# Kernel tuning notes

Measured on AMD Instinct MI355X. Metric: run time of the kernel, lower is better.

The kernel has to match this reference:

```python
import jax, jax.numpy as jnp
import numpy as np

D = 1024      # d_model
H = 16        # num_heads
DK = D // H   # head dim = 64
C = 64        # chunk_size
MRP = 2 * C   # max_rel_pos = 128
B, S = 2, 2048


def setup_inputs() -> dict:
    key = jax.random.key(0)
    ks = jax.random.split(key, 7)
    s = 0.02
    x = jax.random.normal(ks[0], (B, S, D), jnp.float32)
    Wq = jax.random.normal(ks[1], (D, D), jnp.float32) * s
    Wk = jax.random.normal(ks[2], (D, D), jnp.float32) * s
    Wv = jax.random.normal(ks[3], (D, D), jnp.float32) * s
    Wo = jax.random.normal(ks[4], (D, D), jnp.float32) * s
    bq = jnp.zeros((D,), jnp.float32)
    bk = jnp.zeros((D,), jnp.float32)
    bv = jnp.zeros((D,), jnp.float32)
    bo = jnp.zeros((D,), jnp.float32)
    # torch init is zeros; use small values so the bias path is exercised
    rel_bias = jax.random.normal(ks[5], (2 * MRP + 1, H), jnp.float32) * s
    return dict(x=x, Wq=Wq, bq=bq, Wk=Wk, bk=bk, Wv=Wv, bv=bv, Wo=Wo, bo=bo,
                rel_bias=rel_bias)


def reference(x, Wq, bq, Wk, bk, Wv, bv, Wo, bo, rel_bias):
    b, s, _ = x.shape

    def heads(w, bias):
        return (x @ w + bias).reshape(b, s, H, DK).transpose(0, 2, 1, 3)  # [B,H,S,dk]

    Q = heads(Wq, bq)
    K = heads(Wk, bk)
    V = heads(Wv, bv)

    scale = jnp.sqrt(jnp.asarray(DK, x.dtype))
    scores = jnp.einsum('bhqd,bhkd->bhqk', Q, K) / scale  # [B,H,S,S]

    pos = jnp.arange(s)
    # chunked path's rel index reduces to global (q - k), clamped
    rel = jnp.clip(pos[:, None] - pos[None, :], -MRP, MRP) + MRP  # [S,S]
    bias2 = rel_bias[rel].transpose(2, 0, 1)  # [H,S,S]
    scores = scores + bias2[None]

    # growing-window chunk mask: query chunk i sees key chunks 0..i
    qc = pos // C
    allowed = qc[None, :] <= qc[:, None]  # [S_q, S_k]
    scores = jnp.where(allowed[None, None], scores, -jnp.inf)

    attn = jax.nn.softmax(scores, axis=-1)
    out = jnp.einsum('bhqk,bhkd->bhqd', attn, V)
    out = out.transpose(0, 2, 1, 3).reshape(b, s, D)
    return out @ Wo + bo
```

## Files before the change

### kernel.cpp

```cpp
#include <hip/hip_runtime.h>
#include <stdint.h>

#define NH 16
#define DKH 64
#define SEQ 2048
#define NBATCH 2
#define NROW (NBATCH*SEQ)
#define DM 1024
#define LOG2E 1.44269504088896f

typedef __attribute__((ext_vector_type(8))) __bf16 bf16x8;
typedef __attribute__((ext_vector_type(4))) __bf16 bf16x4;
typedef __attribute__((ext_vector_type(4))) float f32x4;

#if __has_builtin(__builtin_amdgcn_exp2f)
#define EXP2(x) __builtin_amdgcn_exp2f(x)
#else
#define EXP2(x) exp2f(x)
#endif

__device__ __forceinline__ unsigned short f2bf(float f) {
  union { float f; uint32_t u; } v; v.f = f;
  uint32_t r = v.u + 0x7FFFu + ((v.u >> 16) & 1u);
  return (unsigned short)(r >> 16);
}
__device__ __forceinline__ f32x4 mfma16(bf16x8 a, bf16x8 b, f32x4 c) {
  return __builtin_amdgcn_mfma_f32_16x16x32_bf16(a, b, c, 0, 0, 0);
}
__device__ __forceinline__ void gload_lds16(const void* g, void* l) {
  __builtin_amdgcn_global_load_lds(
      (__attribute__((address_space(1))) uint32_t*)(uintptr_t)g,
      (__attribute__((address_space(3))) uint32_t*)(uintptr_t)l,
      16, 0, 0);
}
__device__ __forceinline__ void barrier_raw() {
  asm volatile("" ::: "memory");
  __builtin_amdgcn_s_barrier();
  asm volatile("" ::: "memory");
}

__global__ __launch_bounds__(256) void k_cvt_x(const float* __restrict__ x,
                                               unsigned short* __restrict__ xb) {
  int i = blockIdx.x * 256 + threadIdx.x;
  float4 v = ((const float4*)x)[i];
  ushort4 o;
  o.x = f2bf(v.x); o.y = f2bf(v.y); o.z = f2bf(v.z); o.w = f2bf(v.w);
  ((ushort4*)xb)[i] = o;
}

__global__ __launch_bounds__(256) void k_cvt_w(
    const float* __restrict__ Wq, const float* __restrict__ Wk,
    const float* __restrict__ Wv, const float* __restrict__ Wo,
    unsigned short* __restrict__ Wqt, unsigned short* __restrict__ Wkt,
    unsigned short* __restrict__ Wvt, unsigned short* __restrict__ Wot) {
  __shared__ float tile[32][33];
  int z = blockIdx.z;
  const float* W = (z == 0) ? Wq : (z == 1) ? Wk : (z == 2) ? Wv : Wo;
  int ti = blockIdx.x, tj = blockIdx.y;
  int c = threadIdx.x & 31, r0 = threadIdx.x >> 5;
#pragma unroll
  for (int rr = 0; rr < 4; ++rr) {
    int r = r0 + rr * 8;
    tile[r][c] = W[(ti * 32 + r) * DM + tj * 32 + c];
  }
  __syncthreads();
  unsigned short* Out = (z == 0) ? Wqt : (z == 1) ? Wkt : (z == 2) ? Wvt : Wot;
#pragma unroll
  for (int rr = 0; rr < 4; ++rr) {
    int a = r0 + rr * 8;
    float v = tile[c][a];
    Out[(tj * 32 + a) * DM + ti * 32 + c] = f2bf(v);
  }
}

__global__ __launch_bounds__(256) void k_gemm_qkv(
    const unsigned short* __restrict__ xb,
    const unsigned short* __restrict__ Wqt, const unsigned short* __restrict__ Wkt,
    const unsigned short* __restrict__ Wvt,
    const float* __restrict__ bq, const float* __restrict__ bk,
    const float* __restrict__ bv,
    unsigned short* __restrict__ Q, unsigned short* __restrict__ Ko,
    unsigned short* __restrict__ Vt) {
  __shared__ __align__(16) unsigned short Al[2][128 * 64];
  __shared__ __align__(16) unsigned short Bl[2][128 * 64];
  int z = blockIdx.z;
  const unsigned short* Wt = (z == 0) ? Wqt : (z == 1) ? Wkt : Wvt;
  const float* bias = (z == 0) ? bq : (z == 1) ? bk : bv;

  int m0 = blockIdx.x * 128, n0 = blockIdx.y * 128;
  int tid = threadIdx.x, lane = tid & 63, wave = tid >> 6;
  int wr = wave >> 1, wc = wave & 1;
  int l15 = lane & 15, lg = lane >> 4;
  int r3 = lane >> 3, s3 = lane & 7;
  int gsw = (s3 ^ r3) << 4;
  int swz = l15 & 7;

  f32x4 acc[4][4] = {};

  auto stage = [&](int kb, int b) {
#pragma unroll
    for (int c = 0; c < 4; ++c) {
      int rb = c * 32 + wave * 8;
      gload_lds16((const char*)xb + (size_t)(m0 + rb + r3) * 2048 + kb * 128 + gsw,
                  (char*)&Al[b][0] + rb * 128);
      gload_lds16((const char*)Wt + (size_t)(n0 + rb + r3) * 2048 + kb * 128 + gsw,
                  (char*)&Bl[b][0] + rb * 128);
    }
  };

  stage(0, 0);
  stage(1, 1);

  for (int kb = 0; kb < 16; ++kb) {
    if (kb < 15) asm volatile("s_waitcnt vmcnt(8)" ::: "memory");
    else         asm volatile("s_waitcnt vmcnt(0)" ::: "memory");
    barrier_raw();
    int b = kb & 1;
#pragma unroll
    for (int ks = 0; ks < 2; ++ks) {
      int slot = lg + 4 * ks;
      int sofs = ((slot ^ swz) << 4);
      bf16x8 a[4], bfr[4];
#pragma unroll
      for (int mt = 0; mt < 4; ++mt)
        a[mt] = *(const bf16x8*)((const char*)&Al[b][0] + (wr * 64 + mt * 16 + l15) * 128 + sofs);
#pragma unroll
      for (int nt = 0; nt < 4; ++nt)
        bfr[nt] = *(const bf16x8*)((const char*)&Bl[b][0] + (wc * 64 + nt * 16 + l15) * 128 + sofs);
#pragma unroll
      for (int mt = 0; mt < 4; ++mt)
#pragma unroll
        for (int nt = 0; nt < 4; ++nt)
          acc[mt][nt] = mfma16(a[mt], bfr[nt], acc[mt][nt]);
    }
    barrier_raw();
    if (kb < 14) stage(kb + 2, b);
  }

#pragma unroll
  for (int nt = 0; nt < 4; ++nt) {
    int n = n0 + wc * 64 + nt * 16 + l15;
    float bb = bias[n];
    int h = n >> 6, dk = n & 63;
#pragma unroll
    for (int mt = 0; mt < 4; ++mt) {
      int mbase = m0 + wr * 64 + mt * 16 + lg * 4;
      int bidx = mbase >> 11, s = mbase & 2047;
      if (z < 2) {
        unsigned short* Out = (z == 0) ? Q : Ko;
#pragma unroll
        for (int r = 0; r < 4; ++r)
          Out[(((size_t)(bidx * NH + h)) * SEQ + s + r) * DKH + dk] =
              f2bf(acc[mt][nt][r] + bb);
      } else {
        ushort4 pk;
        pk.x = f2bf(acc[mt][nt][0] + bb);
        pk.y = f2bf(acc[mt][nt][1] + bb);
        pk.z = f2bf(acc[mt][nt][2] + bb);
        pk.w = f2bf(acc[mt][nt][3] + bb);
        *(ushort4*)&Vt[((size_t)(bidx * NH + h) * DKH + dk) * SEQ + s] = pk;
      }
    }
  }
}

__global__ __launch_bounds__(256) void k_attn(
    const unsigned short* __restrict__ Qg, const unsigned short* __restrict__ Kg,
    const unsigned short* __restrict__ Vtg, const float* __restrict__ rel_bias,
    unsigned short* __restrict__ AOh) {
  __shared__ __align__(16) unsigned short Kl[2][64 * 64];
  __shared__ __align__(16) unsigned short Vl[2][64 * 64];
  __shared__ float biasl[257];

  int blk = blockIdx.x;
  int bh = blk & 31;
  int g = blk >> 5;
  int qc = (g < 16) ? (31 - g) : (g - 16);
  int h = bh & 15, bidx = bh >> 4;
  int tid = threadIdx.x, lane = tid & 63, wave = tid >> 6;
  int l15 = lane & 15, lg = lane >> 4;
  int r3 = lane >> 3, s3 = lane & 7;
  int gsw = (s3 ^ r3) * 16;

  const float C1L = 0.125f * LOG2E;

  for (int i = tid; i < 257; i += 256)
    biasl[i] = rel_bias[i * NH + h] * LOG2E - 6.0f * LOG2E;

  int qrow = qc * 64 + wave * 16 + l15;
  const unsigned short* qptr = Qg + ((size_t)bh * SEQ + qrow) * DKH + lg * 8;
  bf16x8 qf0 = *(const bf16x8*)(qptr);
  bf16x8 qf1 = *(const bf16x8*)(qptr + 32);

  const char* kcb = (const char*)(Kg + (size_t)bh * SEQ * DKH);
  const char* vcb = (const char*)(Vtg + (size_t)bh * DKH * SEQ);

  auto stage = [&](int j, int b) {
    const char* kj = kcb + (size_t)j * (64 * DKH * 2);
    const char* vj = vcb + (size_t)j * 128;
#pragma unroll
    for (int c = 0; c < 2; ++c) {
      int rb = wave * 16 + c * 8;
      gload_lds16(kj + (size_t)(rb + r3) * 128 + gsw,
                  (char*)&Kl[b][0] + rb * 128);
      gload_lds16(vj + (size_t)(rb + r3) * (SEQ * 2) + gsw,
                  (char*)&Vl[b][0] + rb * 128);
    }
  };

  f32x4 acc[4] = {};
  f32x4 accl = {};
  bf16x8 ones;
#pragma unroll
  for (int jj = 0; jj < 8; ++jj) ones[jj] = (__bf16)1.0f;

  float cfar = rel_bias[256 * NH + h] * LOG2E - 6.0f * LOG2E;
  int swz = (l15 & 7);

  int vo[4];
#pragma unroll
  for (int kt = 0; kt < 4; ++kt)
    vo[kt] = (((kt * 2 + (lg >> 1)) ^ swz) << 4) + ((lg & 1) << 3);

  stage(0, 0);
  asm volatile("s_waitcnt vmcnt(0)" ::: "memory");
  barrier_raw();

  for (int j = 0; j <= qc; ++j) {
    int cur = j & 1;
    if (j < qc) stage(j + 1, cur ^ 1);

    const char* Kc = (const char*)&Kl[cur][0];
    const char* Vc = (const char*)&Vl[cur][0];

    f32x4 sa[4] = {};
    __builtin_amdgcn_s_setprio(1);
#pragma unroll
    for (int ks = 0; ks < 2; ++ks) {
      bf16x8 qa = ks ? qf1 : qf0;
      int slot = lg + 4 * ks;
#pragma unroll
      for (int kt = 0; kt < 4; ++kt) {
        bf16x8 kfr = *(const bf16x8*)(Kc + (kt * 16 + l15) * 128 + ((slot ^ swz) * 16));
        sa[kt] = mfma16(kfr, qa, sa[kt]);
      }
    }
    __builtin_amdgcn_s_setprio(0);

    float p[4][4];
    if (j >= qc - 2) {
      int kb0 = j * 64 + lg * 4;
#pragma unroll
      for (int kt = 0; kt < 4; ++kt)
#pragma unroll
        for (int r = 0; r < 4; ++r) {
          int rel = qrow - (kb0 + kt * 16 + r);
          rel = min(max(rel, -128), 128) + 128;
          p[kt][r] = EXP2(fmaf(sa[kt][r], C1L, biasl[rel]));
        }
    } else {
#pragma unroll
      for (int kt = 0; kt < 4; ++kt)
#pragma unroll
        for (int r = 0; r < 4; ++r)
          p[kt][r] = EXP2(fmaf(sa[kt][r], C1L, cfar));
    }

    bf16x8 pfr0, pfr1;
#pragma unroll
    for (int jj = 0; jj < 4; ++jj) {
      pfr0[jj]     = (__bf16)p[0][jj];
      pfr0[jj + 4] = (__bf16)p[1][jj];
      pfr1[jj]     = (__bf16)p[2][jj];
      pfr1[jj + 4] = (__bf16)p[3][jj];
    }

    __builtin_amdgcn_s_setprio(1);
#pragma unroll
    for (int dt = 0; dt < 4; ++dt) {
      const char* vrow = Vc + (dt * 16 + l15) * 128;
      uint2 t0 = *(const uint2*)(vrow + vo[0]);
      uint2 t1 = *(const uint2*)(vrow + vo[1]);
      uint2 t2 = *(const uint2*)(vrow + vo[2]);
      uint2 t3 = *(const uint2*)(vrow + vo[3]);
      uint4 w0, w1;
      w0.x = t0.x; w0.y = t0.y; w0.z = t1.x; w0.w = t1.y;
      w1.x = t2.x; w1.y = t2.y; w1.z = t3.x; w1.w = t3.y;
      acc[dt] = mfma16(pfr0, *(const bf16x8*)&w0, acc[dt]);
      acc[dt] = mfma16(pfr1, *(const bf16x8*)&w1, acc[dt]);
    }
    accl = mfma16(pfr0, ones, accl);
    accl = mfma16(pfr1, ones, accl);
    __builtin_amdgcn_s_setprio(0);

    if (j < qc) {
      asm volatile("s_waitcnt vmcnt(0)" ::: "memory");
      barrier_raw();
    }
  }

#pragma unroll
  for (int r = 0; r < 4; ++r) {
    float inv = 1.0f / accl[r];
    int s = qc * 64 + wave * 16 + lg * 4 + r;
    size_t row = (size_t)bidx * SEQ + s;
#pragma unroll
    for (int dt = 0; dt < 4; ++dt) {
      float v = acc[dt][r] * inv;
      int col = h * 64 + dt * 16 + l15;
      AOh[row * DM + col] = f2bf(v);
    }
  }
}

__global__ __launch_bounds__(256) void k_gemm_out(
    const unsigned short* __restrict__ Ab, const unsigned short* __restrict__ Bt,
    const float* __restrict__ bo, float* __restrict__ out) {
  __shared__ __align__(16) unsigned short Al[2][64 * 64];
  __shared__ __align__(16) unsigned short Bl[2][128 * 64];

  int m0 = blockIdx.x * 64, n0 = blockIdx.y * 128;
  int tid = threadIdx.x, lane = tid & 63, wave = tid >> 6;
  int wr = wave >> 1, wc = wave & 1;
  int l15 = lane & 15, lg = lane >> 4;
  int r3 = lane >> 3, s3 = lane & 7;
  int gsw = (s3 ^ r3) << 4;
  int swz = l15 & 7;

  f32x4 acc[2][4] = {};

  auto stage = [&](int kb, int b) {
#pragma unroll
    for (int c = 0; c < 2; ++c) {
      int rb = c * 32 + wave * 8;
      gload_lds16((const char*)Ab + (size_t)(m0 + rb + r3) * 2048 + kb * 128 + gsw,
                  (char*)&Al[b][0] + rb * 128);
    }
#pragma unroll
    for (int c = 0; c < 4; ++c) {
      int rb = c * 32 + wave * 8;
      gload_lds16((const char*)Bt + (size_t)(n0 + rb + r3) * 2048 + kb * 128 + gsw,
                  (char*)&Bl[b][0] + rb * 128);
    }
  };

  stage(0, 0);
  stage(1, 1);

  for (int kb = 0; kb < 16; ++kb) {
    if (kb < 15) asm volatile("s_waitcnt vmcnt(6)" ::: "memory");
    else         asm volatile("s_waitcnt vmcnt(0)" ::: "memory");
    barrier_raw();
    int b = kb & 1;
#pragma unroll
    for (int ks = 0; ks < 2; ++ks) {
      int slot = lg + 4 * ks;
      int sofs = ((slot ^ swz) << 4);
      bf16x8 a[2], bfr[4];
#pragma unroll
      for (int mt = 0; mt < 2; ++mt)
        a[mt] = *(const bf16x8*)((const char*)&Al[b][0] + (wr * 32 + mt * 16 + l15) * 128 + sofs);
#pragma unroll
      for (int nt = 0; nt < 4; ++nt)
        bfr[nt] = *(const bf16x8*)((const char*)&Bl[b][0] + (wc * 64 + nt * 16 + l15) * 128 + sofs);
#pragma unroll
      for (int mt = 0; mt < 2; ++mt)
#pragma unroll
        for (int nt = 0; nt < 4; ++nt)
          acc[mt][nt] = mfma16(a[mt], bfr[nt], acc[mt][nt]);
    }
    barrier_raw();
    if (kb < 14) stage(kb + 2, b);
  }

#pragma unroll
  for (int nt = 0; nt < 4; ++nt) {
    int n = n0 + wc * 64 + nt * 16 + l15;
    float bb = bo[n];
#pragma unroll
    for (int mt = 0; mt < 2; ++mt) {
      int mbase = m0 + wr * 32 + mt * 16 + lg * 4;
#pragma unroll
      for (int r = 0; r < 4; ++r)
        out[(size_t)(mbase + r) * DM + n] = acc[mt][nt][r] + bb;
    }
  }
}

extern "C" void kernel_launch(void* const* d_in, const int* in_sizes, int n_in,
                              void* d_out, int out_size, void* d_ws, size_t ws_size,
                              hipStream_t stream) {
  const float* x  = (const float*)d_in[0];
  const float* Wq = (const float*)d_in[1];
  const float* bq = (const float*)d_in[2];
  const float* Wk = (const float*)d_in[3];
  const float* bk = (const float*)d_in[4];
  const float* Wv = (const float*)d_in[5];
  const float* bv = (const float*)d_in[6];
  const float* Wo = (const float*)d_in[7];
  const float* bo = (const float*)d_in[8];
  const float* rb = (const float*)d_in[9];
  float* out = (float*)d_out;

  char* ws = (char*)d_ws;
  size_t off = 0;
  auto alloc = [&](size_t bytes) {
    char* p = ws + off; off += (bytes + 255) & ~(size_t)255; return p;
  };
  unsigned short* xb   = (unsigned short*)alloc((size_t)NROW * DM * 2);
  unsigned short* Wqt  = (unsigned short*)alloc((size_t)DM * DM * 2);
  unsigned short* Wkt  = (unsigned short*)alloc((size_t)DM * DM * 2);
  unsigned short* Wvt  = (unsigned short*)alloc((size_t)DM * DM * 2);
  unsigned short* Wot  = (unsigned short*)alloc((size_t)DM * DM * 2);
  unsigned short* Qb   = (unsigned short*)alloc((size_t)NROW * DM * 2);
  unsigned short* Kb   = (unsigned short*)alloc((size_t)NROW * DM * 2);
  unsigned short* Vtb  = (unsigned short*)alloc((size_t)NROW * DM * 2);
  unsigned short* AOh  = (unsigned short*)alloc((size_t)NROW * DM * 2);

  k_cvt_x<<<dim3(NROW * DM / 4 / 256), dim3(256), 0, stream>>>(x, xb);
  k_cvt_w<<<dim3(32, 32, 4), dim3(256), 0, stream>>>(Wq, Wk, Wv, Wo,
                                                     Wqt, Wkt, Wvt, Wot);
  k_gemm_qkv<<<dim3(32, 8, 3), dim3(256), 0, stream>>>(xb, Wqt, Wkt, Wvt,
                                                       bq, bk, bv, Qb, Kb, Vtb);
  k_attn<<<dim3(1024), dim3(256), 0, stream>>>(Qb, Kb, Vtb, rb, AOh);
  k_gemm_out<<<dim3(64, 8), dim3(256), 0, stream>>>(AOh, Wot, bo, out);
}
```

Before: 100.1 us.

## Process two query chunks per attention block, 32 query rows per wave

Each attention block now covers two adjacent query chunks (128 rows), and each wave handles 32 rows with two fragment sets, so every K/V tile staged into LDS serves twice as many queries. The grid is halved to 512 blocks and uses a new chunk-pair ordering. Waves assigned the lower chunk skip the final key chunk but still take part in the barriers. The cost is more registers per wave, fewer blocks to fill the CUs, and some idle waves on the last iteration.

```diff
diff --git a/kernel.cpp b/kernel.cpp
--- a/kernel.cpp
+++ b/kernel.cpp
@@ -175,22 +175,31 @@
   int blk = blockIdx.x;
   int bh = blk & 31;
   int g = blk >> 5;
-  int qc = (g < 16) ? (31 - g) : (g - 16);
+  int a = (g < 8) ? g : (23 - g);
   int h = bh & 15, bidx = bh >> 4;
-  int tid = threadIdx.x, lane = tid & 63, wave = tid >> 6;
+  int tid = threadIdx.x, lane = tid & 63, w = tid >> 6;
   int l15 = lane & 15, lg = lane >> 4;
   int r3 = lane >> 3, s3 = lane & 7;
   int gsw = (s3 ^ r3) * 16;
 
+  int myqc = 2 * a + (w >> 1);
+  int qsub = w & 1;
+  int qcmax = 2 * a + 1;
+  int qbase = myqc * 64 + qsub * 32;
+
   const float C1L = 0.125f * LOG2E;
 
   for (int i = tid; i < 257; i += 256)
     biasl[i] = rel_bias[i * NH + h] * LOG2E - 6.0f * LOG2E;
 
-  int qrow = qc * 64 + wave * 16 + l15;
-  const unsigned short* qptr = Qg + ((size_t)bh * SEQ + qrow) * DKH + lg * 8;
-  bf16x8 qf0 = *(const bf16x8*)(qptr);
-  bf16x8 qf1 = *(const bf16x8*)(qptr + 32);
+  bf16x8 qf[2][2];
+#pragma unroll
+  for (int f = 0; f < 2; ++f) {
+    const unsigned short* qptr =
+        Qg + ((size_t)bh * SEQ + qbase + f * 16 + l15) * DKH + lg * 8;
+    qf[f][0] = *(const bf16x8*)(qptr);
+    qf[f][1] = *(const bf16x8*)(qptr + 32);
+  }
 
   const char* kcb = (const char*)(Kg + (size_t)bh * SEQ * DKH);
   const char* vcb = (const char*)(Vtg + (size_t)bh * DKH * SEQ);
@@ -200,7 +209,7 @@
     const char* vj = vcb + (size_t)j * 128;
 #pragma unroll
     for (int c = 0; c < 2; ++c) {
-      int rb = wave * 16 + c * 8;
+      int rb = w * 16 + c * 8;
       gload_lds16(kj + (size_t)(rb + r3) * 128 + gsw,
                   (char*)&Kl[b][0] + rb * 128);
       gload_lds16(vj + (size_t)(rb + r3) * (SEQ * 2) + gsw,
@@ -208,8 +217,8 @@
     }
   };
 
-  f32x4 acc[4] = {};
-  f32x4 accl = {};
+  f32x4 acc[2][4] = {};
+  f32x4 accl[2] = {};
   bf16x8 ones;
 #pragma unroll
   for (int jj = 0; jj < 8; ++jj) ones[jj] = (__bf16)1.0f;
@@ -226,91 +235,107 @@
   asm volatile("s_waitcnt vmcnt(0)" ::: "memory");
   barrier_raw();
 
-  for (int j = 0; j <= qc; ++j) {
+  for (int j = 0; j <= qcmax; ++j) {
     int cur = j & 1;
-    if (j < qc) stage(j + 1, cur ^ 1);
-
-    const char* Kc = (const char*)&Kl[cur][0];
-    const char* Vc = (const char*)&Vl[cur][0];
-
-    f32x4 sa[4] = {};
-    __builtin_amdgcn_s_setprio(1);
-#pragma unroll
-    for (int ks = 0; ks < 2; ++ks) {
-      bf16x8 qa = ks ? qf1 : qf0;
-      int slot = lg + 4 * ks;
-#pragma unroll
-      for (int kt = 0; kt < 4; ++kt) {
-        bf16x8 kfr = *(const bf16x8*)(Kc + (kt * 16 + l15) * 128 + ((slot ^ swz) * 16));
-        sa[kt] = mfma16(kfr, qa, sa[kt]);
+    if (j < qcmax) stage(j + 1, cur ^ 1);
+
+    if (j <= myqc) {
+      const char* Kc = (const char*)&Kl[cur][0];
+      const char* Vc = (const char*)&Vl[cur][0];
+
+      f32x4 sa[2][4] = {};
+      __builtin_amdgcn_s_setprio(1);
+#pragma unroll
+      for (int ks = 0; ks < 2; ++ks) {
+        int slot = lg + 4 * ks;
+#pragma unroll
+        for (int kt = 0; kt < 4; ++kt) {
+          bf16x8 kfr = *(const bf16x8*)(Kc + (kt * 16 + l15) * 128 + ((slot ^ swz) * 16));
+          sa[0][kt] = mfma16(kfr, qf[0][ks], sa[0][kt]);
+          sa[1][kt] = mfma16(kfr, qf[1][ks], sa[1][kt]);
+        }
       }
-    }
-    __builtin_amdgcn_s_setprio(0);
-
-    float p[4][4];
-    if (j >= qc - 2) {
-      int kb0 = j * 64 + lg * 4;
-#pragma unroll
-      for (int kt = 0; kt < 4; ++kt)
-#pragma unroll
-        for (int r = 0; r < 4; ++r) {
-          int rel = qrow - (kb0 + kt * 16 + r);
-          rel = min(max(rel, -128), 128) + 128;
-          p[kt][r] = EXP2(fmaf(sa[kt][r], C1L, biasl[rel]));
+      __builtin_amdgcn_s_setprio(0);
+
+      float p[2][4][4];
+      if (j >= myqc - 2) {
+        int kb0 = j * 64 + lg * 4;
+#pragma unroll
+        for (int f = 0; f < 2; ++f) {
+          int qrow = qbase + f * 16 + l15;
+#pragma unroll
+          for (int kt = 0; kt < 4; ++kt)
+#pragma unroll
+            for (int r = 0; r < 4; ++r) {
+              int rel = qrow - (kb0 + kt * 16 + r);
+              rel = min(max(rel, -128), 128) + 128;
+              p[f][kt][r] = EXP2(fmaf(sa[f][kt][r], C1L, biasl[rel]));
+            }
         }
-    } else {
-#pragma unroll
-      for (int kt = 0; kt < 4; ++kt)
-#pragma unroll
-        for (int r = 0; r < 4; ++r)
-          p[kt][r] = EXP2(fmaf(sa[kt][r], C1L, cfar));
-    }
-
-    bf16x8 pfr0, pfr1;
-#pragma unroll
-    for (int jj = 0; jj < 4; ++jj) {
-      pfr0[jj]     = (__bf16)p[0][jj];
-      pfr0[jj + 4] = (__bf16)p[1][jj];
-      pfr1[jj]     = (__bf16)p[2][jj];
-      pfr1[jj + 4] = (__bf16)p[3][jj];
-    }
-
-    __builtin_amdgcn_s_setprio(1);
-#pragma unroll
-    for (int dt = 0; dt < 4; ++dt) {
-      const char* vrow = Vc + (dt * 16 + l15) * 128;
-      uint2 t0 = *(const uint2*)(vrow + vo[0]);
-      uint2 t1 = *(const uint2*)(vrow + vo[1]);
-      uint2 t2 = *(const uint2*)(vrow + vo[2]);
-      uint2 t3 = *(const uint2*)(vrow + vo[3]);
-      uint4 w0, w1;
-      w0.x = t0.x; w0.y = t0.y; w0.z = t1.x; w0.w = t1.y;
-      w1.x = t2.x; w1.y = t2.y; w1.z = t3.x; w1.w = t3.y;
-      acc[dt] = mfma16(pfr0, *(const bf16x8*)&w0, acc[dt]);
-      acc[dt] = mfma16(pfr1, *(const bf16x8*)&w1, acc[dt]);
-    }
-    accl = mfma16(pfr0, ones, accl);
-    accl = mfma16(pfr1, ones, accl);
-    __builtin_amdgcn_s_setprio(0);
-
-    if (j < qc) {
+      } else {
+#pragma unroll
+        for (int f = 0; f < 2; ++f)
+#pragma unroll
+          for (int kt = 0; kt < 4; ++kt)
+#pragma unroll
+            for (int r = 0; r < 4; ++r)
+              p[f][kt][r] = EXP2(fmaf(sa[f][kt][r], C1L, cfar));
+      }
+
+      bf16x8 pfr[2][2];
+#pragma unroll
+      for (int f = 0; f < 2; ++f)
+#pragma unroll
+        for (int jj = 0; jj < 4; ++jj) {
+          pfr[f][0][jj]     = (__bf16)p[f][0][jj];
+          pfr[f][0][jj + 4] = (__bf16)p[f][1][jj];
+          pfr[f][1][jj]     = (__bf16)p[f][2][jj];
+          pfr[f][1][jj + 4] = (__bf16)p[f][3][jj];
+        }
+
+      __builtin_amdgcn_s_setprio(1);
+#pragma unroll
+      for (int dt = 0; dt < 4; ++dt) {
+        const char* vrow = Vc + (dt * 16 + l15) * 128;
+        uint2 t0 = *(const uint2*)(vrow + vo[0]);
+        uint2 t1 = *(const uint2*)(vrow + vo[1]);
+        uint2 t2 = *(const uint2*)(vrow + vo[2]);
+        uint2 t3 = *(const uint2*)(vrow + vo[3]);
+        uint4 w0, w1;
+        w0.x = t0.x; w0.y = t0.y; w0.z = t1.x; w0.w = t1.y;
+        w1.x = t2.x; w1.y = t2.y; w1.z = t3.x; w1.w = t3.y;
+        acc[0][dt] = mfma16(pfr[0][0], *(const bf16x8*)&w0, acc[0][dt]);
+        acc[0][dt] = mfma16(pfr[0][1], *(const bf16x8*)&w1, acc[0][dt]);
+        acc[1][dt] = mfma16(pfr[1][0], *(const bf16x8*)&w0, acc[1][dt]);
+        acc[1][dt] = mfma16(pfr[1][1], *(const bf16x8*)&w1, acc[1][dt]);
+      }
+      accl[0] = mfma16(pfr[0][0], ones, accl[0]);
+      accl[0] = mfma16(pfr[0][1], ones, accl[0]);
+      accl[1] = mfma16(pfr[1][0], ones, accl[1]);
+      accl[1] = mfma16(pfr[1][1], ones, accl[1]);
+      __builtin_amdgcn_s_setprio(0);
+    }
+
+    if (j < qcmax) {
       asm volatile("s_waitcnt vmcnt(0)" ::: "memory");
       barrier_raw();
     }
   }
 
 #pragma unroll
-  for (int r = 0; r < 4; ++r) {
-    float inv = 1.0f / accl[r];
-    int s = qc * 64 + wave * 16 + lg * 4 + r;
-    size_t row = (size_t)bidx * SEQ + s;
-#pragma unroll
-    for (int dt = 0; dt < 4; ++dt) {
-      float v = acc[dt][r] * inv;
-      int col = h * 64 + dt * 16 + l15;
-      AOh[row * DM + col] = f2bf(v);
-    }
-  }
+  for (int f = 0; f < 2; ++f)
+#pragma unroll
+    for (int r = 0; r < 4; ++r) {
+      float inv = 1.0f / accl[f][r];
+      int s = qbase + f * 16 + lg * 4 + r;
+      size_t row = (size_t)bidx * SEQ + s;
+#pragma unroll
+      for (int dt = 0; dt < 4; ++dt) {
+        float v = acc[f][dt][r] * inv;
+        int col = h * 64 + dt * 16 + l15;
+        AOh[row * DM + col] = f2bf(v);
+      }
+    }
 }
 
 __global__ __launch_bounds__(256) void k_gemm_out(
@@ -422,6 +447,6 @@
                                                      Wqt, Wkt, Wvt, Wot);
   k_gemm_qkv<<<dim3(32, 8, 3), dim3(256), 0, stream>>>(xb, Wqt, Wkt, Wvt,
                                                        bq, bk, bv, Qb, Kb, Vtb);
-  k_attn<<<dim3(1024), dim3(256), 0, stream>>>(Qb, Kb, Vtb, rb, AOh);
+  k_attn<<<dim3(512), dim3(256), 0, stream>>>(Qb, Kb, Vtb, rb, AOh);
   k_gemm_out<<<dim3(64, 8), dim3(256), 0, stream>>>(AOh, Wot, bo, out);
 }
```

Result: slower. 113.6 us (+13.4%).
